# Performance work log

Hardware: AMD Instinct MI355X
Metric: run time of the kernel (lower is better)

The kernel has to match this reference:

```python
import jax, jax.numpy as jnp
import numpy as np

N_NODES = 50000
N_EDGES = 1_600_000
IN_CH = 128
HID = 128


def setup_inputs() -> dict:
    key = jax.random.key(0)
    ks = jax.random.split(key, 8)
    x = jax.random.normal(ks[0], (N_NODES, IN_CH), dtype=jnp.float32)
    edge_index = jax.random.randint(ks[1], (2, N_EDGES), 0, N_NODES, dtype=jnp.int64)
    def glorot(k, shape):
        fan_in, fan_out = shape
        s = jnp.sqrt(6.0 / (fan_in + fan_out))
        return jax.random.uniform(k, shape, jnp.float32, -s, s)
    return {
        "x": x,
        "edge_index": edge_index,
        "W1": glorot(ks[2], (IN_CH, HID)), "b1": jnp.zeros((HID,), jnp.float32),
        "W2": glorot(ks[3], (HID, HID)), "b2": jnp.zeros((HID,), jnp.float32),
        "W_age": glorot(ks[4], (HID, 3)), "b_age": jnp.zeros((3,), jnp.float32),
        "W_sex": glorot(ks[5], (HID, 2)), "b_sex": jnp.zeros((2,), jnp.float32),
        "W_eth": glorot(ks[6], (HID, 3)), "b_eth": jnp.zeros((3,), jnp.float32),
    }


def _prep_graph(edge_index, n_nodes):
    # PyG GCNConv default: add self-loops, symmetric normalization.
    loops = jnp.arange(n_nodes, dtype=edge_index.dtype)
    src = jnp.concatenate([edge_index[0], loops])
    dst = jnp.concatenate([edge_index[1], loops])
    deg = jax.ops.segment_sum(jnp.ones_like(dst, jnp.float32), dst, num_segments=n_nodes)
    dinv = jnp.where(deg > 0, jax.lax.rsqrt(deg), 0.0)
    norm = dinv[src] * dinv[dst]  # [E+N]
    return src, dst, norm


def _gcn_conv(x, W, b, src, dst, norm, n_nodes):
    h = x @ W                              # [N, out] linear transform first
    msg = h[src] * norm[:, None]           # gather + normalize
    out = jax.ops.segment_sum(msg, dst, num_segments=n_nodes)  # scatter-add
    return out + b


def reference(x, edge_index, W1, b1, W2, b2, W_age, b_age, W_sex, b_sex, W_eth, b_eth):
    n = x.shape[0]
    src, dst, norm = _prep_graph(edge_index, n)
    h = jax.nn.relu(_gcn_conv(x, W1, b1, src, dst, norm, n))
    h = jax.nn.relu(_gcn_conv(h, W2, b2, src, dst, norm, n))
    age = _gcn_conv(h, W_age, b_age, src, dst, norm, n)
    sex = _gcn_conv(h, W_sex, b_sex, src, dst, norm, n)
    eth = _gcn_conv(h, W_eth, b_eth, src, dst, norm, n)
    return age, sex, eth
```

## Files before the change

kernel.cpp:

```cpp
#include <hip/hip_runtime.h>
#include <hip/hip_fp16.h>


#define NBUK_MAX 512

typedef float vfloat2 __attribute__((ext_vector_type(2)));

__global__ __launch_bounds__(256) void k_bhist(const int* __restrict__ dst, int E, int nbuk,
                                               int* __restrict__ bcount) {
    __shared__ int h[NBUK_MAX];
    int tid = threadIdx.x;
    for (int i = tid; i < nbuk; i += 256) h[i] = 0;
    __syncthreads();
    int s0 = blockIdx.x * 4096;
#pragma unroll
    for (int i = 0; i < 16; i++) {
        int e = s0 + i * 256 + tid;
        if (e < E) atomicAdd(&h[dst[e] >> 7], 1);
    }
    __syncthreads();
    for (int i = tid; i < nbuk; i += 256)
        if (h[i]) atomicAdd(&bcount[i], h[i]);
}

__global__ __launch_bounds__(512) void k_bscan(const int* __restrict__ bcount, int nb,
                                               int* __restrict__ bbase, int* __restrict__ bcur) {
    __shared__ int s[512];
    int tid = threadIdx.x;
    int v = (tid < nb) ? bcount[tid] : 0;
    s[tid] = v;
    __syncthreads();
    for (int off = 1; off < 512; off <<= 1) {
        int t = (tid >= off) ? s[tid - off] : 0;
        __syncthreads();
        s[tid] += t;
        __syncthreads();
    }
    if (tid < nb) {
        int excl = s[tid] - v;
        bbase[tid] = excl;
        bcur[tid] = excl;
        if (tid == nb - 1) bbase[nb] = s[tid];
    }
}

__global__ __launch_bounds__(256) void k_passA(const int* __restrict__ src,
                                               const int* __restrict__ dst, int E, int nbuk,
                                               int* __restrict__ bcur,
                                               unsigned* __restrict__ bbuf) {
    __shared__ int h[NBUK_MAX];
    __shared__ int base[NBUK_MAX];
    __shared__ int lcur[NBUK_MAX];
    int tid = threadIdx.x;
    for (int i = tid; i < nbuk; i += 256) h[i] = 0;
    __syncthreads();
    int s0 = blockIdx.x * 4096;
#pragma unroll
    for (int i = 0; i < 16; i++) {
        int e = s0 + i * 256 + tid;
        if (e < E) atomicAdd(&h[dst[e] >> 7], 1);
    }
    __syncthreads();
    for (int i = tid; i < nbuk; i += 256) {
        int c = h[i];
        base[i] = c ? atomicAdd(&bcur[i], c) : 0;
        lcur[i] = 0;
    }
    __syncthreads();
#pragma unroll
    for (int i = 0; i < 16; i++) {
        int e = s0 + i * 256 + tid;
        if (e < E) {
            int d = dst[e];
            int b = d >> 7;
            int idx = atomicAdd(&lcur[b], 1);
            bbuf[base[b] + idx] = ((unsigned)d << 16) | (unsigned)src[e];
        }
    }
}

__global__ __launch_bounds__(256) void k_passB(const unsigned* __restrict__ bbuf,
                                               const int* __restrict__ bbase, int N,
                                               int* __restrict__ row_ptr,
                                               float* __restrict__ dinv,
                                               unsigned short* __restrict__ sorted) {
    __shared__ int h[128], sc[128], lc[128];
    int b = blockIdx.x, tid = threadIdx.x;
    int node0 = b << 7;
    int ncnt = min(128, N - node0);
    int s = bbase[b], e = bbase[b + 1];
    if (tid < 128) h[tid] = 0;
    __syncthreads();
    for (int i = s + tid; i < e; i += 256) atomicAdd(&h[(bbuf[i] >> 16) & 127], 1);
    __syncthreads();
    if (tid < 128) sc[tid] = h[tid];
    __syncthreads();
    for (int off = 1; off < 128; off <<= 1) {
        int t = 0;
        if (tid < 128 && tid >= off) t = sc[tid - off];
        __syncthreads();
        if (tid < 128) sc[tid] += t;
        __syncthreads();
    }
    if (tid < ncnt) {
        int excl = sc[tid] - h[tid];
        row_ptr[node0 + tid] = s + excl;
        dinv[node0 + tid] = rsqrtf((float)(h[tid] + 1));
        lc[tid] = excl;
    }
    if (b == gridDim.x - 1 && tid == 0) row_ptr[N] = e;
    __syncthreads();
    for (int i = s + tid; i < e; i += 256) {
        unsigned p = bbuf[i];
        int nl = (p >> 16) & 127;
        int idx = atomicAdd(&lc[nl], 1);
        sorted[s + idx] = (unsigned short)(p & 0xffffu);
    }
}

__global__ __launch_bounds__(256) void k_gemm_scale_h(const float* __restrict__ in,
                                                      const float* __restrict__ W,
                                                      const float* __restrict__ dinv, int N,
                                                      __half* __restrict__ out) {
    __shared__ float Ws[32][128];
    __shared__ float Xs[32][64];
    int tid = threadIdx.x;
    int row0 = blockIdx.x * 64;
    int tc = tid & 15;
    int tr = tid >> 4;
    float acc[4][8];
#pragma unroll
    for (int i = 0; i < 4; i++)
#pragma unroll
        for (int j = 0; j < 8; j++) acc[i][j] = 0.f;

    for (int k0 = 0; k0 < 128; k0 += 32) {
#pragma unroll
        for (int j = 0; j < 4; j++) {
            int u = tid + j * 256;
            int kk = u >> 5, c4 = u & 31;
            *(float4*)&Ws[kk][c4 * 4] = *(const float4*)&W[(k0 + kk) * 128 + c4 * 4];
        }
#pragma unroll
        for (int j = 0; j < 2; j++) {
            int u = tid + j * 256;
            int r = u >> 3, kq = u & 7;
            int row = row0 + r;
            if (row > N - 1) row = N - 1;
            float4 v = *(const float4*)&in[(size_t)row * 128 + k0 + kq * 4];
            Xs[kq * 4 + 0][r] = v.x;
            Xs[kq * 4 + 1][r] = v.y;
            Xs[kq * 4 + 2][r] = v.z;
            Xs[kq * 4 + 3][r] = v.w;
        }
        __syncthreads();
#pragma unroll 8
        for (int kk = 0; kk < 32; kk++) {
            float4 xv = *(const float4*)&Xs[kk][tr * 4];
            float4 wa = *(const float4*)&Ws[kk][tc * 8];
            float4 wb = *(const float4*)&Ws[kk][tc * 8 + 4];
            float xr[4] = {xv.x, xv.y, xv.z, xv.w};
            float wc[8] = {wa.x, wa.y, wa.z, wa.w, wb.x, wb.y, wb.z, wb.w};
#pragma unroll
            for (int i = 0; i < 4; i++)
#pragma unroll
                for (int j = 0; j < 8; j++) acc[i][j] += xr[i] * wc[j];
        }
        __syncthreads();
    }
#pragma unroll
    for (int i = 0; i < 4; i++) {
        int row = row0 + tr * 4 + i;
        if (row < N) {
            float di = dinv[row];
            union {
                uint4 u;
                __half h[8];
            } pk;
#pragma unroll
            for (int j = 0; j < 8; j++) pk.h[j] = __float2half_rn(di * acc[i][j]);
            *(uint4*)&out[(size_t)row * 128 + tc * 8] = pk.u;
        }
    }
}

__global__ __launch_bounds__(256) void k_agg128h(const __half* __restrict__ hs,
                                                 const int* __restrict__ row_ptr,
                                                 const unsigned short* __restrict__ ss,
                                                 const float* __restrict__ dinv,
                                                 const float* __restrict__ bias, int N,
                                                 int do_relu, float* __restrict__ out) {
    int wid = threadIdx.x >> 6;
    int lane = threadIdx.x & 63;
    int node = blockIdx.x * 4 + wid;
    if (node >= N) return;
    const __half2* hp = (const __half2*)hs;
    float2 acc = __half22float2(hp[(size_t)node * 64 + lane]);
    int s = row_ptr[node], e = row_ptr[node + 1];
    int i = s;
    for (; i + 8 <= e; i += 8) {
        int id[8];
#pragma unroll
        for (int u = 0; u < 8; u++) id[u] = __builtin_nontemporal_load(&ss[i + u]);
        float2 v[8];
#pragma unroll
        for (int u = 0; u < 8; u++) v[u] = __half22float2(hp[(size_t)id[u] * 64 + lane]);
        float sx0 = (v[0].x + v[1].x) + (v[2].x + v[3].x);
        float sx1 = (v[4].x + v[5].x) + (v[6].x + v[7].x);
        float sy0 = (v[0].y + v[1].y) + (v[2].y + v[3].y);
        float sy1 = (v[4].y + v[5].y) + (v[6].y + v[7].y);
        acc.x += sx0 + sx1;
        acc.y += sy0 + sy1;
    }
    for (; i < e; i++) {
        float2 v0 = __half22float2(hp[(size_t)ss[i] * 64 + lane]);
        acc.x += v0.x;
        acc.y += v0.y;
    }
    float di = dinv[node];
    int c = lane * 2;
    float2 b = *(const float2*)&bias[c];
    float ox = di * acc.x + b.x;
    float oy = di * acc.y + b.y;
    if (do_relu) {
        ox = fmaxf(ox, 0.f);
        oy = fmaxf(oy, 0.f);
    }
    vfloat2 o;
    o.x = ox;
    o.y = oy;
    __builtin_nontemporal_store(o, (vfloat2*)&out[(size_t)node * 128 + c]);
}

__global__ __launch_bounds__(256) void k_headgemm(const float* __restrict__ h,
                                                  const float* __restrict__ Wa,
                                                  const float* __restrict__ Wsx,
                                                  const float* __restrict__ We,
                                                  const float* __restrict__ dinv, int N,
                                                  float* __restrict__ ths) {
    __shared__ float Ws8[128][8];
    int tid = threadIdx.x;
#pragma unroll
    for (int j = 0; j < 4; j++) {
        int u = tid + j * 256;
        int k = u >> 3, c = u & 7;
        float v;
        if (c < 3) v = Wa[k * 3 + c];
        else if (c < 5) v = Wsx[k * 2 + (c - 3)];
        else v = We[k * 3 + (c - 5)];
        Ws8[k][c] = v;
    }
    __syncthreads();
    int node = blockIdx.x * 32 + (tid >> 3);
    int col = tid & 7;
    if (node >= N) return;
    const float* hr = &h[(size_t)node * 128];
    float acc = 0.f;
#pragma unroll 4
    for (int k = 0; k < 128; k += 4) {
        float4 hv = *(const float4*)&hr[k];
        acc += hv.x * Ws8[k][col] + hv.y * Ws8[k + 1][col] + hv.z * Ws8[k + 2][col] +
               hv.w * Ws8[k + 3][col];
    }
    ths[(size_t)node * 8 + col] = dinv[node] * acc;
}

__global__ __launch_bounds__(256) void k_agg8(const float* __restrict__ ths,
                                              const int* __restrict__ row_ptr,
                                              const unsigned short* __restrict__ ss,
                                              const float* __restrict__ dinv,
                                              const float* __restrict__ ba,
                                              const float* __restrict__ bs,
                                              const float* __restrict__ be, int N,
                                              float* __restrict__ outp) {
    int tid = threadIdx.x;
    int node = blockIdx.x * 32 + (tid >> 3);
    int j = tid & 7;
    if (node >= N) return;
    float acc = ths[(size_t)node * 8 + j];
    int s = row_ptr[node], e = row_ptr[node + 1];
    for (int i = s; i < e; i++) {
        int sc = ss[i];
        acc += ths[(size_t)sc * 8 + j];
    }
    float bias = (j < 3) ? ba[j] : ((j < 5) ? bs[j - 3] : be[j - 5]);
    float v = dinv[node] * acc + bias;
    if (j < 3) outp[(size_t)node * 3 + j] = v;
    else if (j < 5) outp[(size_t)N * 3 + (size_t)node * 2 + (j - 3)] = v;
    else outp[(size_t)N * 5 + (size_t)node * 3 + (j - 5)] = v;
}

extern "C" void kernel_launch(void* const* d_in, const int* in_sizes, int n_in,
                              void* d_out, int out_size, void* d_ws, size_t ws_size,
                              hipStream_t stream) {
    const float* x = (const float*)d_in[0];
    const int* edge = (const int*)d_in[1];
    const float* W1 = (const float*)d_in[2];
    const float* b1 = (const float*)d_in[3];
    const float* W2 = (const float*)d_in[4];
    const float* b2 = (const float*)d_in[5];
    const float* Wa = (const float*)d_in[6];
    const float* ba = (const float*)d_in[7];
    const float* Wsx = (const float*)d_in[8];
    const float* bs = (const float*)d_in[9];
    const float* We = (const float*)d_in[10];
    const float* be = (const float*)d_in[11];

    int N = in_sizes[0] / 128;
    int E = in_sizes[1] / 2;
    const int* srcp = edge;
    const int* dstp = edge + E;
    int nbuk = (N + 127) >> 7;

    char* ws = (char*)d_ws;
    size_t off = 0;
    auto alloc = [&](size_t bytes) -> char* {
        char* p = ws + off;
        off += (bytes + 255) & ~(size_t)255;
        return p;
    };
    int* bcount = (int*)alloc((size_t)(nbuk + 1) * 4);
    int* bbase = (int*)alloc((size_t)(nbuk + 1) * 4);
    int* bcur = (int*)alloc((size_t)(nbuk + 1) * 4);
    int* row_ptr = (int*)alloc((size_t)(N + 1) * 4);
    float* dinv = (float*)alloc((size_t)N * 4);
    unsigned* bbuf = (unsigned*)alloc((size_t)E * 4);
    unsigned short* sorted = (unsigned short*)alloc((size_t)E * 2);
    __half* bufH = (__half*)alloc((size_t)N * 128 * 2);
    float* bufF = (float*)alloc((size_t)N * 128 * 4);
    float* ths = (float*)alloc((size_t)N * 8 * 4);

    int nbT = (E + 4095) / 4096;

    hipMemsetAsync(bcount, 0, (size_t)(nbuk + 1) * 4, stream);
    k_bhist<<<nbT, 256, 0, stream>>>(dstp, E, nbuk, bcount);
    k_bscan<<<1, 512, 0, stream>>>(bcount, nbuk, bbase, bcur);
    k_passA<<<nbT, 256, 0, stream>>>(srcp, dstp, E, nbuk, bcur, bbuf);
    k_passB<<<nbuk, 256, 0, stream>>>(bbuf, bbase, N, row_ptr, dinv, sorted);

    int gb = (N + 63) / 64;
    k_gemm_scale_h<<<gb, 256, 0, stream>>>(x, W1, dinv, N, bufH);
    k_agg128h<<<(N + 3) / 4, 256, 0, stream>>>(bufH, row_ptr, sorted, dinv, b1, N, 1, bufF);
    k_gemm_scale_h<<<gb, 256, 0, stream>>>(bufF, W2, dinv, N, bufH);
    k_agg128h<<<(N + 3) / 4, 256, 0, stream>>>(bufH, row_ptr, sorted, dinv, b2, N, 1, bufF);
    k_headgemm<<<(N + 31) / 32, 256, 0, stream>>>(bufF, Wa, Wsx, We, dinv, N, ths);
    k_agg8<<<(N + 31) / 32, 256, 0, stream>>>(ths, row_ptr, sorted, dinv, ba, bs, be, N,
                                              (float*)d_out);
}
```

Baseline: 279.0 us.

## Use split-fp16 MFMA for the 128x128 GEMMs and retune the sort and aggregate launches

The FP32 shared-memory tiled GEMM is replaced by an MFMA 16x16x32 f16 kernel. It keeps roughly FP32 accuracy by splitting both operands into high and low fp16 parts and summing three products. A small pre-kernel transposes and splits the weights. The edge-bucketing kernels now process 8192 edges per block instead of 4096. The aggregation kernel runs one 64-thread block per node and uses a plain store instead of a nontemporal one. The new GEMM writes scattered 2-byte outputs and reads weights straight from global memory, and the split-fp16 scheme adds some rounding risk.

```diff
diff --git a/kernel.cpp b/kernel.cpp
--- a/kernel.cpp
+++ b/kernel.cpp
@@ -3,8 +3,10 @@
 
 
 #define NBUK_MAX 512
-
-typedef float vfloat2 __attribute__((ext_vector_type(2)));
+#define EPB 8192
+
+typedef _Float16 f16x8 __attribute__((ext_vector_type(8)));
+typedef float f32x4 __attribute__((ext_vector_type(4)));
 
 __global__ __launch_bounds__(256) void k_bhist(const int* __restrict__ dst, int E, int nbuk,
                                                int* __restrict__ bcount) {
@@ -12,9 +14,9 @@
     int tid = threadIdx.x;
     for (int i = tid; i < nbuk; i += 256) h[i] = 0;
     __syncthreads();
-    int s0 = blockIdx.x * 4096;
-#pragma unroll
-    for (int i = 0; i < 16; i++) {
+    int s0 = blockIdx.x * EPB;
+#pragma unroll
+    for (int i = 0; i < EPB / 256; i++) {
         int e = s0 + i * 256 + tid;
         if (e < E) atomicAdd(&h[dst[e] >> 7], 1);
     }
@@ -54,9 +56,9 @@
     int tid = threadIdx.x;
     for (int i = tid; i < nbuk; i += 256) h[i] = 0;
     __syncthreads();
-    int s0 = blockIdx.x * 4096;
-#pragma unroll
-    for (int i = 0; i < 16; i++) {
+    int s0 = blockIdx.x * EPB;
+#pragma unroll
+    for (int i = 0; i < EPB / 256; i++) {
         int e = s0 + i * 256 + tid;
         if (e < E) atomicAdd(&h[dst[e] >> 7], 1);
     }
@@ -68,7 +70,7 @@
     }
     __syncthreads();
 #pragma unroll
-    for (int i = 0; i < 16; i++) {
+    for (int i = 0; i < EPB / 256; i++) {
         int e = s0 + i * 256 + tid;
         if (e < E) {
             int d = dst[e];
@@ -118,81 +120,87 @@
     }
 }
 
-__global__ __launch_bounds__(256) void k_gemm_scale_h(const float* __restrict__ in,
-                                                      const float* __restrict__ W,
-                                                      const float* __restrict__ dinv, int N,
-                                                      __half* __restrict__ out) {
-    __shared__ float Ws[32][128];
-    __shared__ float Xs[32][64];
-    int tid = threadIdx.x;
-    int row0 = blockIdx.x * 64;
-    int tc = tid & 15;
-    int tr = tid >> 4;
-    float acc[4][8];
-#pragma unroll
-    for (int i = 0; i < 4; i++)
-#pragma unroll
-        for (int j = 0; j < 8; j++) acc[i][j] = 0.f;
-
-    for (int k0 = 0; k0 < 128; k0 += 32) {
-#pragma unroll
-        for (int j = 0; j < 4; j++) {
-            int u = tid + j * 256;
-            int kk = u >> 5, c4 = u & 31;
-            *(float4*)&Ws[kk][c4 * 4] = *(const float4*)&W[(k0 + kk) * 128 + c4 * 4];
-        }
-#pragma unroll
-        for (int j = 0; j < 2; j++) {
-            int u = tid + j * 256;
-            int r = u >> 3, kq = u & 7;
-            int row = row0 + r;
-            if (row > N - 1) row = N - 1;
-            float4 v = *(const float4*)&in[(size_t)row * 128 + k0 + kq * 4];
-            Xs[kq * 4 + 0][r] = v.x;
-            Xs[kq * 4 + 1][r] = v.y;
-            Xs[kq * 4 + 2][r] = v.z;
-            Xs[kq * 4 + 3][r] = v.w;
-        }
-        __syncthreads();
-#pragma unroll 8
-        for (int kk = 0; kk < 32; kk++) {
-            float4 xv = *(const float4*)&Xs[kk][tr * 4];
-            float4 wa = *(const float4*)&Ws[kk][tc * 8];
-            float4 wb = *(const float4*)&Ws[kk][tc * 8 + 4];
-            float xr[4] = {xv.x, xv.y, xv.z, xv.w};
-            float wc[8] = {wa.x, wa.y, wa.z, wa.w, wb.x, wb.y, wb.z, wb.w};
-#pragma unroll
-            for (int i = 0; i < 4; i++)
-#pragma unroll
-                for (int j = 0; j < 8; j++) acc[i][j] += xr[i] * wc[j];
-        }
-        __syncthreads();
-    }
-#pragma unroll
-    for (int i = 0; i < 4; i++) {
-        int row = row0 + tr * 4 + i;
-        if (row < N) {
-            float di = dinv[row];
-            union {
-                uint4 u;
-                __half h[8];
-            } pk;
-#pragma unroll
-            for (int j = 0; j < 8; j++) pk.h[j] = __float2half_rn(di * acc[i][j]);
-            *(uint4*)&out[(size_t)row * 128 + tc * 8] = pk.u;
-        }
-    }
-}
-
-__global__ __launch_bounds__(256) void k_agg128h(const __half* __restrict__ hs,
-                                                 const int* __restrict__ row_ptr,
-                                                 const unsigned short* __restrict__ ss,
-                                                 const float* __restrict__ dinv,
-                                                 const float* __restrict__ bias, int N,
-                                                 int do_relu, float* __restrict__ out) {
+__global__ __launch_bounds__(64) void k_wsplit(const float* __restrict__ W,
+                                               __half* __restrict__ wth,
+                                               __half* __restrict__ wtl) {
+    int t = blockIdx.x * 64 + threadIdx.x;
+#pragma unroll
+    for (int u = 0; u < 8; u++) {
+        int idx = t * 8 + u;
+        int k = idx >> 7, c = idx & 127;
+        float w = W[k * 128 + c];
+        _Float16 h = (_Float16)w;
+        _Float16 l = (_Float16)(w - (float)h);
+        wth[c * 128 + k] = *(__half*)&h;
+        wtl[c * 128 + k] = *(__half*)&l;
+    }
+}
+
+__global__ __launch_bounds__(256) void k_gemm_mfma(const float* __restrict__ in,
+                                                   const __half* __restrict__ wth,
+                                                   const __half* __restrict__ wtl,
+                                                   const float* __restrict__ dinv, int N,
+                                                   __half* __restrict__ out) {
     int wid = threadIdx.x >> 6;
     int lane = threadIdx.x & 63;
-    int node = blockIdx.x * 4 + wid;
+    int row0 = blockIdx.x * 64 + wid * 16;
+    int lr = lane & 15;
+    int lk = (lane >> 4) * 8;
+
+    f16x8 ah[4], al[4];
+    int arow = row0 + lr;
+    if (arow > N - 1) arow = N - 1;
+    const float* xr = &in[(size_t)arow * 128];
+#pragma unroll
+    for (int ks = 0; ks < 4; ks++) {
+        float4 a0 = *(const float4*)&xr[ks * 32 + lk];
+        float4 a1 = *(const float4*)&xr[ks * 32 + lk + 4];
+        float av[8] = {a0.x, a0.y, a0.z, a0.w, a1.x, a1.y, a1.z, a1.w};
+#pragma unroll
+        for (int j = 0; j < 8; j++) {
+            _Float16 h = (_Float16)av[j];
+            ah[ks][j] = h;
+            al[ks][j] = (_Float16)(av[j] - (float)h);
+        }
+    }
+    float dv[4];
+#pragma unroll
+    for (int i = 0; i < 4; i++) {
+        int r = row0 + (lane >> 4) * 4 + i;
+        dv[i] = dinv[min(r, N - 1)];
+    }
+
+#pragma unroll
+    for (int ct = 0; ct < 8; ct++) {
+        f32x4 acc = {0.f, 0.f, 0.f, 0.f};
+        int c = ct * 16 + lr;
+#pragma unroll
+        for (int ks = 0; ks < 4; ks++) {
+            f16x8 bh = *(const f16x8*)&wth[(size_t)c * 128 + ks * 32 + lk];
+            f16x8 bl = *(const f16x8*)&wtl[(size_t)c * 128 + ks * 32 + lk];
+            acc = __builtin_amdgcn_mfma_f32_16x16x32_f16(ah[ks], bh, acc, 0, 0, 0);
+            acc = __builtin_amdgcn_mfma_f32_16x16x32_f16(al[ks], bh, acc, 0, 0, 0);
+            acc = __builtin_amdgcn_mfma_f32_16x16x32_f16(ah[ks], bl, acc, 0, 0, 0);
+        }
+#pragma unroll
+        for (int i = 0; i < 4; i++) {
+            int r = row0 + (lane >> 4) * 4 + i;
+            if (r < N) {
+                _Float16 hv = (_Float16)(dv[i] * acc[i]);
+                out[(size_t)r * 128 + ct * 16 + lr] = *(__half*)&hv;
+            }
+        }
+    }
+}
+
+__global__ __launch_bounds__(64) void k_agg128h(const __half* __restrict__ hs,
+                                                const int* __restrict__ row_ptr,
+                                                const unsigned short* __restrict__ ss,
+                                                const float* __restrict__ dinv,
+                                                const float* __restrict__ bias, int N,
+                                                int do_relu, float* __restrict__ out) {
+    int lane = threadIdx.x;
+    int node = blockIdx.x;
     if (node >= N) return;
     const __half2* hp = (const __half2*)hs;
     float2 acc = __half22float2(hp[(size_t)node * 64 + lane]);
@@ -226,10 +234,7 @@
         ox = fmaxf(ox, 0.f);
         oy = fmaxf(oy, 0.f);
     }
-    vfloat2 o;
-    o.x = ox;
-    o.y = oy;
-    __builtin_nontemporal_store(o, (vfloat2*)&out[(size_t)node * 128 + c]);
+    *(float2*)&out[(size_t)node * 128 + c] = {ox, oy};
 }
 
 __global__ __launch_bounds__(256) void k_headgemm(const float* __restrict__ h,
@@ -329,20 +334,26 @@
     __half* bufH = (__half*)alloc((size_t)N * 128 * 2);
     float* bufF = (float*)alloc((size_t)N * 128 * 4);
     float* ths = (float*)alloc((size_t)N * 8 * 4);
-
-    int nbT = (E + 4095) / 4096;
+    __half* w1th = (__half*)alloc(128 * 128 * 2);
+    __half* w1tl = (__half*)alloc(128 * 128 * 2);
+    __half* w2th = (__half*)alloc(128 * 128 * 2);
+    __half* w2tl = (__half*)alloc(128 * 128 * 2);
+
+    int nbT = (E + EPB - 1) / EPB;
 
     hipMemsetAsync(bcount, 0, (size_t)(nbuk + 1) * 4, stream);
     k_bhist<<<nbT, 256, 0, stream>>>(dstp, E, nbuk, bcount);
     k_bscan<<<1, 512, 0, stream>>>(bcount, nbuk, bbase, bcur);
     k_passA<<<nbT, 256, 0, stream>>>(srcp, dstp, E, nbuk, bcur, bbuf);
     k_passB<<<nbuk, 256, 0, stream>>>(bbuf, bbase, N, row_ptr, dinv, sorted);
+    k_wsplit<<<32, 64, 0, stream>>>(W1, w1th, w1tl);
+    k_wsplit<<<32, 64, 0, stream>>>(W2, w2th, w2tl);
 
     int gb = (N + 63) / 64;
-    k_gemm_scale_h<<<gb, 256, 0, stream>>>(x, W1, dinv, N, bufH);
-    k_agg128h<<<(N + 3) / 4, 256, 0, stream>>>(bufH, row_ptr, sorted, dinv, b1, N, 1, bufF);
-    k_gemm_scale_h<<<gb, 256, 0, stream>>>(bufF, W2, dinv, N, bufH);
-    k_agg128h<<<(N + 3) / 4, 256, 0, stream>>>(bufH, row_ptr, sorted, dinv, b2, N, 1, bufF);
+    k_gemm_mfma<<<gb, 256, 0, stream>>>(x, w1th, w1tl, dinv, N, bufH);
+    k_agg128h<<<N, 64, 0, stream>>>(bufH, row_ptr, sorted, dinv, b1, N, 1, bufF);
+    k_gemm_mfma<<<gb, 256, 0, stream>>>(bufF, w2th, w2tl, dinv, N, bufH);
+    k_agg128h<<<N, 64, 0, stream>>>(bufH, row_ptr, sorted, dinv, b2, N, 1, bufF);
     k_headgemm<<<(N + 31) / 32, 256, 0, stream>>>(bufF, Wa, Wsx, We, dinv, N, ths);
     k_agg8<<<(N + 31) / 32, 256, 0, stream>>>(ths, row_ptr, sorted, dinv, ba, bs, be, N,
                                               (float*)d_out);
```

Result: slower. 294.1 us (+5.4%).
